# Performance work log

Hardware: AMD Instinct MI355X
Metric: run time of the kernel (lower is better)

## Reference

```python
import jax, jax.numpy as jnp
import numpy as np

SIZE = 64
B, NMAX = 8, 24


def setup_inputs() -> dict:
    key = jax.random.key(0)
    ks = jax.random.split(key, 8)
    # valid boxes: top-left in [0,400), width/height in [10,210)
    xy = jax.random.uniform(ks[0], (B, NMAX, 2)) * 400.0
    wh = jax.random.uniform(ks[1], (B, NMAX, 2)) * 200.0 + 10.0
    bboxes = jnp.concatenate([xy, xy + wh], axis=-1)  # [B,N,4] (x1,y1,x2,y2)
    num_obj = jax.random.randint(ks[2], (B,), 2, NMAX + 1)
    conv1_w = jax.random.normal(ks[3], (64, 2, 5, 5)) * 0.1
    conv1_b = jnp.zeros((64,), jnp.float32)
    conv2_w = jax.random.normal(ks[4], (32, 64, 5, 5)) * 0.05
    conv2_b = jnp.zeros((32,), jnp.float32)
    lin_w = jax.random.normal(ks[5], (5408, 4800)) * 0.01
    lin_b = jnp.zeros((4800,), jnp.float32)
    return dict(bboxes=bboxes, num_obj=num_obj, conv1_w=conv1_w, conv1_b=conv1_b,
                conv2_w=conv2_w, conv2_b=conv2_b, lin_w=lin_w, lin_b=lin_b)


def _pair_indices(num_obj):
    # ragged pair construction on host; num_obj is an integer constant input
    n = np.asarray(num_obj)
    bs, is_, js = [], [], []
    for b in range(n.shape[0]):
        ii, jj = np.triu_indices(int(n[b]), k=1)
        bs.append(np.full(ii.shape, b, dtype=np.int32))
        is_.append(ii.astype(np.int32))
        js.append(jj.astype(np.int32))
    return np.concatenate(bs), np.concatenate(is_), np.concatenate(js)


def _get_sp(boxA, boxB):
    # DRG-style spatial map: rescale both boxes into the union-box frame
    # (aspect preserving, shorter axis centered), rasterize as binary masks.
    # boxA, boxB: [M,4] -> [M,2,64,64]
    u1 = jnp.minimum(boxA[:, 0], boxB[:, 0])
    v1 = jnp.minimum(boxA[:, 1], boxB[:, 1])
    u2 = jnp.maximum(boxA[:, 2], boxB[:, 2])
    v2 = jnp.maximum(boxA[:, 3], boxB[:, 3])
    w = u2 - u1
    h = v2 - v1
    scale = (SIZE - 1.0) / jnp.maximum(jnp.maximum(w, h), 1e-6)
    offx = jnp.where(h >= w, (SIZE - 1.0 - w * scale) * 0.5, 0.0)
    offy = jnp.where(w > h, (SIZE - 1.0 - h * scale) * 0.5, 0.0)

    xs = jnp.arange(SIZE, dtype=jnp.float32)[None, None, :]
    ys = jnp.arange(SIZE, dtype=jnp.float32)[None, :, None]

    def rast(box):
        x1 = jnp.round((box[:, 0] - u1) * scale + offx)[:, None, None]
        y1 = jnp.round((box[:, 1] - v1) * scale + offy)[:, None, None]
        x2 = jnp.round((box[:, 2] - u1) * scale + offx)[:, None, None]
        y2 = jnp.round((box[:, 3] - v1) * scale + offy)[:, None, None]
        m = (xs >= x1) & (xs <= x2) & (ys >= y1) & (ys <= y2)
        return m.astype(jnp.float32)

    return jnp.stack([rast(boxA), rast(boxB)], axis=1)


def _conv(x, w, b):
    y = jax.lax.conv_general_dilated(x, w, (1, 1), 'VALID',
                                     dimension_numbers=('NCHW', 'OIHW', 'NCHW'))
    return y + b[None, :, None, None]


def _pool(x):
    return jax.lax.reduce_window(x, -jnp.inf, jax.lax.max,
                                 (1, 1, 2, 2), (1, 1, 2, 2), 'VALID')


def reference(bboxes, num_obj, conv1_w, conv1_b, conv2_w, conv2_b, lin_w, lin_b):
    bi, ii, ji = _pair_indices(num_obj)
    boxA = bboxes[bi, ii]                       # [M,4]
    boxB = bboxes[bi, ji]                       # [M,4]
    sp = _get_sp(boxA, boxB)                    # [M,2,64,64]
    x = jax.nn.relu(_conv(sp, conv1_w, conv1_b))   # [M,64,60,60]
    x = _pool(x)                                   # [M,64,30,30]
    x = jax.nn.relu(_conv(x, conv2_w, conv2_b))    # [M,32,26,26]
    x = _pool(x)                                   # [M,32,13,13]
    x = x.reshape(x.shape[0], -1)                  # [M,5408]
    feat = jax.nn.relu(x @ lin_w + lin_b)          # [M,4800]
    slicing = jnp.stack([jnp.asarray(bi), jnp.asarray(ii), jnp.asarray(ji)],
                        axis=1).astype(jnp.float32)  # [M,3]
    return feat, slicing
```

## Files before the change

### kernel.cpp

```cpp
#include <hip/hip_runtime.h>
#include <hip/hip_bf16.h>

typedef __attribute__((ext_vector_type(8))) short short8;
typedef __attribute__((ext_vector_type(4))) float f32x4;

__device__ inline unsigned short f2bf(float x) {
  unsigned u = __float_as_uint(x);
  unsigned rounding = 0x7FFFu + ((u >> 16) & 1u);
  return (unsigned short)((u + rounding) >> 16);
}
__device__ inline float bf2f(unsigned short u) {
  return __uint_as_float(((unsigned)u) << 16);
}
__device__ inline void gload_lds16(const void* g, void* l) {
  __builtin_amdgcn_global_load_lds(
      (const __attribute__((address_space(1))) unsigned int*)g,
      (__attribute__((address_space(3))) unsigned int*)l, 16, 0, 0);
}

#define KPAD 5440
#define NPAD 4864

__global__ void prep_pairs(const float* __restrict__ bboxes,
                           const int* __restrict__ num_obj, int M,
                           int* __restrict__ pairTab,
                           float* __restrict__ slicing) {
  __shared__ int cum[9];
  if (threadIdx.x == 0) {
    int c = 0; cum[0] = 0;
    for (int b = 0; b < 8; b++) { int n = num_obj[b]; c += n*(n-1)/2; cum[b+1] = c; }
  }
  __syncthreads();
  for (int m = threadIdx.x; m < M; m += blockDim.x) {
    int b = 0;
    while (b < 7 && m >= cum[b+1]) b++;
    int p = m - cum[b];
    int n = num_obj[b];
    int i = 0, rem = p;
    while (rem >= (n - 1 - i)) { rem -= (n - 1 - i); i++; }
    int j = i + 1 + rem;
    const float* A = bboxes + (b*24 + i)*4;
    const float* Bb = bboxes + (b*24 + j)*4;
    float ax1=A[0], ay1=A[1], ax2=A[2], ay2=A[3];
    float bx1=Bb[0], by1=Bb[1], bx2=Bb[2], by2=Bb[3];
    float u1 = fminf(ax1,bx1), v1 = fminf(ay1,by1);
    float u2 = fmaxf(ax2,bx2), v2 = fmaxf(ay2,by2);
    float w = u2-u1, h = v2-v1;
    float scale = 63.0f / fmaxf(fmaxf(w,h), 1e-6f);
    float offx = (h >= w) ? __fmul_rn(63.0f - __fmul_rn(w,scale), 0.5f) : 0.0f;
    float offy = (w > h)  ? __fmul_rn(63.0f - __fmul_rn(h,scale), 0.5f) : 0.0f;
    int* t = pairTab + m*8;
    t[0] = (int)rintf(__fadd_rn(__fmul_rn(ax1-u1, scale), offx));
    t[1] = (int)rintf(__fadd_rn(__fmul_rn(ay1-v1, scale), offy));
    t[2] = (int)rintf(__fadd_rn(__fmul_rn(ax2-u1, scale), offx));
    t[3] = (int)rintf(__fadd_rn(__fmul_rn(ay2-v1, scale), offy));
    t[4] = (int)rintf(__fadd_rn(__fmul_rn(bx1-u1, scale), offx));
    t[5] = (int)rintf(__fadd_rn(__fmul_rn(by1-v1, scale), offy));
    t[6] = (int)rintf(__fadd_rn(__fmul_rn(bx2-u1, scale), offx));
    t[7] = (int)rintf(__fadd_rn(__fmul_rn(by2-v1, scale), offy));
    slicing[m*3+0] = (float)b;
    slicing[m*3+1] = (float)i;
    slicing[m*3+2] = (float)j;
  }
}

__global__ void prep_tables(const float* __restrict__ w1, const float* __restrict__ w2,
                            float* __restrict__ T, unsigned short* __restrict__ W2A) {
  int idx = blockIdx.x*256 + threadIdx.x;
  if (idx < 86528) {
    int o = idx & 63;
    int t = idx >> 6;
    int rxi = t % 26; t /= 26;
    int ryi = t % 26;
    int c = t / 26;
    int ky0 = ryi/5, ky1 = ryi%5, kx0 = rxi/5, kx1 = rxi%5;
    float s = 0.f;
    for (int ky = ky0; ky <= ky1; ky++)
      for (int kx = kx0; kx <= kx1; kx++)
        s += w1[((o*2 + c)*5 + ky)*5 + kx];
    T[idx] = s;
  } else if (idx < 86528 + 51200) {
    int i = idx - 86528;
    int j = i & 7, ln = (i>>3) & 63;
    int mtk = i >> 9;
    int mt = mtk & 1, kk = mtk >> 1;
    int oc = mt*16 + (ln & 15);
    int k = kk*32 + ((ln>>4)<<3) + j;
    int halfk = k/800, r = k%800;
    int kyx = r >> 5, icl = r & 31;
    int ic = halfk*32 + icl, ky = kyx/5, kx = kyx%5;
    W2A[i] = f2bf(w2[((oc*64 + ic)*5 + ky)*5 + kx]);
  }
}

__global__ __launch_bounds__(256) void prep_wt(const float* __restrict__ lw,
                                               unsigned short* __restrict__ Wt) {
  __shared__ unsigned short tile[64][65];
  int k0 = blockIdx.x*64, n0 = blockIdx.y*64;
  for (int i = threadIdx.x; i < 64*64; i += 256) {
    int r = i >> 6, cdx = i & 63;
    int k = k0 + r, n = n0 + cdx;
    float v = (k < 5408) ? lw[(size_t)k*4800 + n] : 0.f;
    tile[r][cdx] = f2bf(v);
  }
  __syncthreads();
  for (int i = threadIdx.x; i < 64*64; i += 256) {
    int r = i >> 6, cdx = i & 63;
    int n = n0 + r, k = k0 + cdx;
    Wt[(size_t)n*KPAD + k] = tile[cdx][r];
  }
}

__global__ __launch_bounds__(256) void pair_conv(
    const int* __restrict__ pairTab, const float* __restrict__ T,
    const unsigned short* __restrict__ W2A, const float* __restrict__ b1,
    const float* __restrict__ b2, unsigned short* __restrict__ X) {
  __shared__ unsigned short p1[28800];
  __shared__ unsigned char rIdx[4][64];
  int m = blockIdx.x;
  int tid = threadIdx.x, lane = tid & 63, wid = tid >> 6;
  const int* pt = pairTab + m*8;

  if (tid < 240) {
    int q = tid % 60, which = tid / 60;
    int lo, hi;
    if (which == 0)      { lo = pt[1]; hi = pt[3]; }
    else if (which == 1) { lo = pt[5]; hi = pt[7]; }
    else if (which == 2) { lo = pt[0]; hi = pt[2]; }
    else                 { lo = pt[4]; hi = pt[6]; }
    int k0 = lo - q; if (k0 < 0) k0 = 0;
    int k1 = hi - q; if (k1 > 4) k1 = 4;
    rIdx[which][q] = (k0 > k1) ? (unsigned char)25 : (unsigned char)(k0*5 + k1);
  }

  int rowbase[11];
#pragma unroll
  for (int tt = 0; tt < 11; tt++) {
    int pos = (wid*11 + tt)*16 + (lane & 15);
    if (pos > 675) pos = 675;
    rowbase[tt] = (pos/26)*30 + (pos % 26);
  }
  f32x4 acc[11][2];
#pragma unroll
  for (int tt = 0; tt < 11; tt++) {
    acc[tt][0] = (f32x4){0.f,0.f,0.f,0.f};
    acc[tt][1] = (f32x4){0.f,0.f,0.f,0.f};
  }

  int icgl = lane >> 4;
  for (int half = 0; half < 2; half++) {
    __syncthreads();
    for (int item = tid; item < 3600; item += 256) {
      int pos = item >> 2;
      int icg = item & 3;
      int ic0 = half*32 + icg*8;
      int py = pos / 30, px = pos % 30;
      float best[8];
#pragma unroll
      for (int j = 0; j < 8; j++) best[j] = -1e30f;
#pragma unroll
      for (int d = 0; d < 4; d++) {
        int y = py*2 + (d>>1), x = px*2 + (d&1);
        int rya = rIdx[0][y], ryb = rIdx[1][y];
        int rxa = rIdx[2][x], rxb = rIdx[3][x];
        const float* Ta = T + (((rya)*26 + rxa)<<6) + ic0;
        const float* Tb = T + (((26 + ryb)*26 + rxb)<<6) + ic0;
        f32x4 a0 = *(const f32x4*)Ta, a1 = *(const f32x4*)(Ta+4);
        f32x4 c0 = *(const f32x4*)Tb, c1 = *(const f32x4*)(Tb+4);
#pragma unroll
        for (int j = 0; j < 4; j++) {
          best[j]   = fmaxf(best[j],   a0[j]+c0[j]);
          best[4+j] = fmaxf(best[4+j], a1[j]+c1[j]);
        }
      }
      short8 v;
#pragma unroll
      for (int j = 0; j < 8; j++)
        v[j] = (short)f2bf(fmaxf(best[j] + b1[ic0+j], 0.f));
      int byte = pos*64 + ((icg ^ ((pos>>1)&3))<<4);
      *(short8*)((char*)p1 + byte) = v;
    }
    __syncthreads();
    for (int kl = 0; kl < 25; kl++) {
      int kk = half*25 + kl;
      const unsigned short* wptr = W2A + ((size_t)(kk*2)*64 + lane)*8;
      short8 a0 = *(const short8*)wptr;
      short8 a1 = *(const short8*)(wptr + 512);
      int radd = (kl/5)*30 + (kl%5);
#pragma unroll
      for (int tt = 0; tt < 11; tt++) {
        int row = rowbase[tt] + radd;
        int byte = row*64 + ((icgl ^ ((row>>1)&3))<<4);
        short8 bv = *(const short8*)((const char*)p1 + byte);
        acc[tt][0] = __builtin_amdgcn_mfma_f32_16x16x32_bf16(a0, bv, acc[tt][0], 0, 0, 0);
        acc[tt][1] = __builtin_amdgcn_mfma_f32_16x16x32_bf16(a1, bv, acc[tt][1], 0, 0, 0);
      }
    }
  }
  __syncthreads();
#pragma unroll
  for (int tt = 0; tt < 11; tt++) {
    int pos = (wid*11 + tt)*16 + (lane & 15);
    if (pos <= 675) {
#pragma unroll
      for (int mt = 0; mt < 2; mt++)
#pragma unroll
        for (int r = 0; r < 4; r++) {
          int oc = mt*16 + ((lane>>4)<<2) + r;
          p1[oc*676 + pos] = f2bf(acc[tt][mt][r]);
        }
    }
  }
  __syncthreads();
  for (int f = tid; f < KPAD; f += 256) {
    unsigned short outv = 0;
    if (f < 5408) {
      int oc = f / 169, rem = f % 169;
      int py = rem / 13, px = rem % 13;
      const unsigned short* c2 = p1 + oc*676 + py*52 + px*2;
      float v = fmaxf(fmaxf(bf2f(c2[0]), bf2f(c2[1])), fmaxf(bf2f(c2[26]), bf2f(c2[27])));
      outv = f2bf(fmaxf(v + b2[oc], 0.f));
    }
    X[(size_t)m*KPAD + f] = outv;
  }
}

__global__ __launch_bounds__(256) void gemm_lin(
    const unsigned short* __restrict__ X, const unsigned short* __restrict__ Wt,
    const float* __restrict__ lin_b, float* __restrict__ P, float* __restrict__ out,
    int M, int Mpad, int splits) {
  __shared__ unsigned short As[2][4096];
  __shared__ unsigned short Bs[2][8192];
  int tid = threadIdx.x, lane = tid & 63, wid = tid >> 6;
  int m0 = blockIdx.x * 64, n0 = blockIdx.y * 128;
  int ks = blockIdx.z;
  int itBeg = (ks * 85) / splits, itEnd = ((ks + 1) * 85) / splits;
  int wm = wid >> 1, wn = wid & 1;

  f32x4 acc[2][4];
#pragma unroll
  for (int i = 0; i < 2; i++)
#pragma unroll
    for (int j = 0; j < 4; j++) acc[i][j] = (f32x4){0.f,0.f,0.f,0.f};

  int rsub = lane >> 3;
  int kslot = (lane & 7) ^ rsub;
  int kg = lane >> 4;

  auto stage = [&](int buf, int it) {
    size_t kof = (size_t)it * 64 + kslot * 8;
#pragma unroll
    for (int cc = 0; cc < 2; cc++) {
      int chunk = wid + cc*4;
      int gm = m0 + chunk*8 + rsub;
      gload_lds16(X + (size_t)gm*KPAD + kof, (char*)As[buf] + chunk*1024);
    }
#pragma unroll
    for (int cc = 0; cc < 4; cc++) {
      int chunk = wid + cc*4;
      int gn = n0 + chunk*8 + rsub;
      gload_lds16(Wt + (size_t)gn*KPAD + kof, (char*)Bs[buf] + chunk*1024);
    }
  };

  stage(0, itBeg);
  __syncthreads();
  int cur = 0;
  for (int it = itBeg; it < itEnd; ++it) {
    if (it + 1 < itEnd) stage(cur ^ 1, it + 1);
#pragma unroll
    for (int ksub = 0; ksub < 2; ++ksub) {
      int slot = ksub*4 + kg;
      short8 af[2], bfr[4];
#pragma unroll
      for (int mf = 0; mf < 2; mf++) {
        int r = wm*32 + mf*16 + (lane & 15);
        af[mf] = *(const short8*)((const char*)As[cur] + r*128 + ((slot ^ (lane&7))<<4));
      }
#pragma unroll
      for (int nf = 0; nf < 4; nf++) {
        int r = wn*64 + nf*16 + (lane & 15);
        bfr[nf] = *(const short8*)((const char*)Bs[cur] + r*128 + ((slot ^ (lane&7))<<4));
      }
#pragma unroll
      for (int mf = 0; mf < 2; mf++)
#pragma unroll
        for (int nf = 0; nf < 4; nf++)
          acc[mf][nf] = __builtin_amdgcn_mfma_f32_16x16x32_bf16(af[mf], bfr[nf], acc[mf][nf], 0, 0, 0);
    }
    __syncthreads();
    cur ^= 1;
  }

  if (splits == 1) {
#pragma unroll
    for (int mf = 0; mf < 2; mf++)
#pragma unroll
      for (int nf = 0; nf < 4; nf++) {
        int n = n0 + wn*64 + nf*16 + (lane & 15);
#pragma unroll
        for (int r = 0; r < 4; r++) {
          int mm = m0 + wm*32 + mf*16 + ((lane>>4)<<2) + r;
          if (mm < M && n < 4800)
            out[(size_t)mm*4800 + n] = fmaxf(acc[mf][nf][r] + lin_b[n], 0.f);
        }
      }
  } else {
    float* Pp = P + (size_t)ks * Mpad * NPAD;
#pragma unroll
    for (int mf = 0; mf < 2; mf++)
#pragma unroll
      for (int nf = 0; nf < 4; nf++) {
        int n = n0 + wn*64 + nf*16 + (lane & 15);
#pragma unroll
        for (int r = 0; r < 4; r++) {
          int mm = m0 + wm*32 + mf*16 + ((lane>>4)<<2) + r;
          Pp[(size_t)mm*NPAD + n] = acc[mf][nf][r];
        }
      }
  }
}

__global__ void reduce_out(const float* __restrict__ P, const float* __restrict__ lb,
                           float* __restrict__ out, int M, int Mpad, int splits) {
  int total = M * 1200;
  for (int idx = blockIdx.x*256 + threadIdx.x; idx < total; idx += gridDim.x*256) {
    int m = idx / 1200, q = idx - m*1200;
    int n = q * 4;
    f32x4 s = *(const f32x4*)(P + (size_t)m*NPAD + n);
    for (int sidx = 1; sidx < splits; sidx++)
      s += *(const f32x4*)(P + (size_t)sidx*Mpad*NPAD + (size_t)m*NPAD + n);
    f32x4 b = *(const f32x4*)(lb + n);
    f32x4 r;
#pragma unroll
    for (int j = 0; j < 4; j++) r[j] = fmaxf(s[j] + b[j], 0.f);
    *(f32x4*)(out + (size_t)m*4800 + n) = r;
  }
}

extern "C" void kernel_launch(void* const* d_in, const int* in_sizes, int n_in,
                              void* d_out, int out_size, void* d_ws, size_t ws_size,
                              hipStream_t stream) {
  const float* bboxes = (const float*)d_in[0];
  const int*   num_obj = (const int*)d_in[1];
  const float* w1 = (const float*)d_in[2];
  const float* b1 = (const float*)d_in[3];
  const float* w2 = (const float*)d_in[4];
  const float* b2 = (const float*)d_in[5];
  const float* lw = (const float*)d_in[6];
  const float* lb = (const float*)d_in[7];
  float* out = (float*)d_out;
  int M = out_size / 4803;
  int Mpad = (M + 63) & ~63;

  size_t fixed = 0;
  auto align512 = [](size_t x) { return (x + 511) & ~(size_t)511; };
  fixed += align512((size_t)M*8*4);
  fixed += align512((size_t)86528*4);
  fixed += align512((size_t)51200*2);
  fixed += align512((size_t)4800*KPAD*2);
  fixed += align512((size_t)Mpad*KPAD*2);
  int splits = 4;
  while (splits > 1 && fixed + align512((size_t)splits*Mpad*NPAD*4) > ws_size) splits >>= 1;

  char* ws = (char*)d_ws;
  size_t off = 0;
  auto alloc = [&](size_t bytes) {
    off = align512(off);
    char* p = ws + off;
    off += bytes;
    return p;
  };
  int* pairTab = (int*)alloc((size_t)M*8*4);
  float* T = (float*)alloc((size_t)86528*4);
  unsigned short* W2A = (unsigned short*)alloc((size_t)51200*2);
  unsigned short* Wt = (unsigned short*)alloc((size_t)4800*KPAD*2);
  unsigned short* X = (unsigned short*)alloc((size_t)Mpad*KPAD*2);
  float* P = (splits > 1) ? (float*)alloc((size_t)splits*Mpad*NPAD*4) : nullptr;

  prep_pairs<<<1, 256, 0, stream>>>(bboxes, num_obj, M, pairTab, out + (size_t)M*4800);
  prep_tables<<<(137728+255)/256, 256, 0, stream>>>(w1, w2, T, W2A);
  prep_wt<<<dim3(85, 75), 256, 0, stream>>>(lw, Wt);
  pair_conv<<<M, 256, 0, stream>>>(pairTab, T, W2A, b1, b2, X);
  gemm_lin<<<dim3(Mpad/64, 38, splits), 256, 0, stream>>>(X, Wt, lb, P, out, M, Mpad, splits);
  if (splits > 1)
    reduce_out<<<1024, 256, 0, stream>>>(P, lb, out, M, Mpad, splits);
}
```

Baseline: 278.7 us.

## Halve pair_conv LDS by processing conv2 input channels in four 16-channel passes

Result: slower. 472.8 us (+69.7%).

```diff
diff --git a/kernel.cpp b/kernel.cpp
--- a/kernel.cpp
+++ b/kernel.cpp
@@ -65,7 +65,7 @@
 }
 
 __global__ void prep_tables(const float* __restrict__ w1, const float* __restrict__ w2,
-                            float* __restrict__ T, unsigned short* __restrict__ W2A) {
+                            float* __restrict__ T, unsigned short* __restrict__ W2B) {
   int idx = blockIdx.x*256 + threadIdx.x;
   if (idx < 86528) {
     int o = idx & 63;
@@ -79,17 +79,22 @@
       for (int kx = kx0; kx <= kx1; kx++)
         s += w1[((o*2 + c)*5 + ky)*5 + kx];
     T[idx] = s;
-  } else if (idx < 86528 + 51200) {
+  } else if (idx < 86528 + 53248) {
     int i = idx - 86528;
-    int j = i & 7, ln = (i>>3) & 63;
-    int mtk = i >> 9;
-    int mt = mtk & 1, kk = mtk >> 1;
+    int j = i & 7;
+    int ln = (i >> 3) & 63;
+    int r1 = i >> 9;
+    int mt = r1 & 1;
+    int r2 = r1 >> 1;
+    int s = r2 % 13;
+    int pp = r2 / 13;
     int oc = mt*16 + (ln & 15);
-    int k = kk*32 + ((ln>>4)<<3) + j;
-    int halfk = k/800, r = k%800;
-    int kyx = r >> 5, icl = r & 31;
-    int ic = halfk*32 + icl, ky = kyx/5, kx = kyx%5;
-    W2A[i] = f2bf(w2[((oc*64 + ic)*5 + ky)*5 + kx]);
+    int q = ln >> 4;
+    int kyx = 2*s + (q >> 1);
+    int ic = pp*16 + ((q & 1) << 3) + j;
+    float val = 0.f;
+    if (kyx < 25) val = w2[((oc*64 + ic)*5 + kyx/5)*5 + (kyx%5)];
+    W2B[i] = f2bf(val);
   }
 }
 
@@ -111,11 +116,11 @@
   }
 }
 
-__global__ __launch_bounds__(256) void pair_conv(
+__global__ __launch_bounds__(256, 4) void pair_conv(
     const int* __restrict__ pairTab, const float* __restrict__ T,
-    const unsigned short* __restrict__ W2A, const float* __restrict__ b1,
+    const unsigned short* __restrict__ W2B, const float* __restrict__ b1,
     const float* __restrict__ b2, unsigned short* __restrict__ X) {
-  __shared__ unsigned short p1[28800];
+  __shared__ unsigned short p1[14400];
   __shared__ unsigned char rIdx[4][64];
   int m = blockIdx.x;
   int tid = threadIdx.x, lane = tid & 63, wid = tid >> 6;
@@ -147,13 +152,16 @@
     acc[tt][1] = (f32x4){0.f,0.f,0.f,0.f};
   }
 
-  int icgl = lane >> 4;
-  for (int half = 0; half < 2; half++) {
-    __syncthreads();
-    for (int item = tid; item < 3600; item += 256) {
-      int pos = item >> 2;
-      int icg = item & 3;
-      int ic0 = half*32 + icg*8;
+  int q = lane >> 4;
+  int qh = q >> 1;
+  int qs = q & 1;
+
+  for (int pp = 0; pp < 4; pp++) {
+    __syncthreads();
+    for (int item = tid; item < 1800; item += 256) {
+      int pos = item >> 1;
+      int icg = item & 1;
+      int ch0 = pp*16 + icg*8;
       int py = pos / 30, px = pos % 30;
       float best[8];
 #pragma unroll
@@ -163,8 +171,8 @@
         int y = py*2 + (d>>1), x = px*2 + (d&1);
         int rya = rIdx[0][y], ryb = rIdx[1][y];
         int rxa = rIdx[2][x], rxb = rIdx[3][x];
-        const float* Ta = T + (((rya)*26 + rxa)<<6) + ic0;
-        const float* Tb = T + (((26 + ryb)*26 + rxb)<<6) + ic0;
+        const float* Ta = T + (((rya)*26 + rxa)<<6) + ch0;
+        const float* Tb = T + (((26 + ryb)*26 + rxb)<<6) + ch0;
         f32x4 a0 = *(const f32x4*)Ta, a1 = *(const f32x4*)(Ta+4);
         f32x4 c0 = *(const f32x4*)Tb, c1 = *(const f32x4*)(Tb+4);
 #pragma unroll
@@ -176,53 +184,53 @@
       short8 v;
 #pragma unroll
       for (int j = 0; j < 8; j++)
-        v[j] = (short)f2bf(fmaxf(best[j] + b1[ic0+j], 0.f));
-      int byte = pos*64 + ((icg ^ ((pos>>1)&3))<<4);
+        v[j] = (short)f2bf(fmaxf(best[j] + b1[ch0+j], 0.f));
+      int byte = pos*32 + ((icg ^ ((pos>>2)&1))<<4);
       *(short8*)((char*)p1 + byte) = v;
     }
     __syncthreads();
-    for (int kl = 0; kl < 25; kl++) {
-      int kk = half*25 + kl;
-      const unsigned short* wptr = W2A + ((size_t)(kk*2)*64 + lane)*8;
+    const unsigned short* wbase = W2B + (size_t)(pp*13)*1024;
+    for (int s = 0; s < 13; s++) {
+      const unsigned short* wptr = wbase + (size_t)s*1024 + lane*8;
       short8 a0 = *(const short8*)wptr;
       short8 a1 = *(const short8*)(wptr + 512);
-      int radd = (kl/5)*30 + (kl%5);
+      int kyx = 2*s + qh; if (kyx > 24) kyx = 24;
+      int radd = (kyx/5)*30 + (kyx%5);
 #pragma unroll
       for (int tt = 0; tt < 11; tt++) {
         int row = rowbase[tt] + radd;
-        int byte = row*64 + ((icgl ^ ((row>>1)&3))<<4);
+        int byte = row*32 + ((qs ^ ((row>>2)&1))<<4);
         short8 bv = *(const short8*)((const char*)p1 + byte);
         acc[tt][0] = __builtin_amdgcn_mfma_f32_16x16x32_bf16(a0, bv, acc[tt][0], 0, 0, 0);
         acc[tt][1] = __builtin_amdgcn_mfma_f32_16x16x32_bf16(a1, bv, acc[tt][1], 0, 0, 0);
       }
     }
   }
-  __syncthreads();
-#pragma unroll
-  for (int tt = 0; tt < 11; tt++) {
-    int pos = (wid*11 + tt)*16 + (lane & 15);
-    if (pos <= 675) {
-#pragma unroll
-      for (int mt = 0; mt < 2; mt++)
+  for (int mt = 0; mt < 2; mt++) {
+    __syncthreads();
+#pragma unroll
+    for (int tt = 0; tt < 11; tt++) {
+      int pos = (wid*11 + tt)*16 + (lane & 15);
+      if (pos <= 675) {
 #pragma unroll
         for (int r = 0; r < 4; r++) {
-          int oc = mt*16 + ((lane>>4)<<2) + r;
-          p1[oc*676 + pos] = f2bf(acc[tt][mt][r]);
+          int ocl = (q<<2) + r;
+          p1[ocl*676 + pos] = f2bf(acc[tt][mt][r]);
         }
-    }
-  }
-  __syncthreads();
-  for (int f = tid; f < KPAD; f += 256) {
-    unsigned short outv = 0;
-    if (f < 5408) {
-      int oc = f / 169, rem = f % 169;
+      }
+    }
+    __syncthreads();
+    for (int f = tid; f < 2704; f += 256) {
+      int ocl = f / 169, rem = f % 169;
+      int oc = mt*16 + ocl;
       int py = rem / 13, px = rem % 13;
-      const unsigned short* c2 = p1 + oc*676 + py*52 + px*2;
+      const unsigned short* c2 = p1 + ocl*676 + py*52 + px*2;
       float v = fmaxf(fmaxf(bf2f(c2[0]), bf2f(c2[1])), fmaxf(bf2f(c2[26]), bf2f(c2[27])));
-      outv = f2bf(fmaxf(v + b2[oc], 0.f));
-    }
-    X[(size_t)m*KPAD + f] = outv;
-  }
+      X[(size_t)m*KPAD + oc*169 + rem] = f2bf(fmaxf(v + b2[oc], 0.f));
+    }
+  }
+  for (int f = 5408 + tid; f < KPAD; f += 256)
+    X[(size_t)m*KPAD + f] = 0;
 }
 
 __global__ __launch_bounds__(256) void gemm_lin(
@@ -325,8 +333,8 @@
                            float* __restrict__ out, int M, int Mpad, int splits) {
   int total = M * 1200;
   for (int idx = blockIdx.x*256 + threadIdx.x; idx < total; idx += gridDim.x*256) {
-    int m = idx / 1200, q = idx - m*1200;
-    int n = q * 4;
+    int m = idx / 1200, qq = idx - m*1200;
+    int n = qq * 4;
     f32x4 s = *(const f32x4*)(P + (size_t)m*NPAD + n);
     for (int sidx = 1; sidx < splits; sidx++)
       s += *(const f32x4*)(P + (size_t)sidx*Mpad*NPAD + (size_t)m*NPAD + n);
@@ -357,7 +365,7 @@
   auto align512 = [](size_t x) { return (x + 511) & ~(size_t)511; };
   fixed += align512((size_t)M*8*4);
   fixed += align512((size_t)86528*4);
-  fixed += align512((size_t)51200*2);
+  fixed += align512((size_t)53248*2);
   fixed += align512((size_t)4800*KPAD*2);
   fixed += align512((size_t)Mpad*KPAD*2);
   int splits = 4;
@@ -373,15 +381,15 @@
   };
   int* pairTab = (int*)alloc((size_t)M*8*4);
   float* T = (float*)alloc((size_t)86528*4);
-  unsigned short* W2A = (unsigned short*)alloc((size_t)51200*2);
+  unsigned short* W2B = (unsigned short*)alloc((size_t)53248*2);
   unsigned short* Wt = (unsigned short*)alloc((size_t)4800*KPAD*2);
   unsigned short* X = (unsigned short*)alloc((size_t)Mpad*KPAD*2);
   float* P = (splits > 1) ? (float*)alloc((size_t)splits*Mpad*NPAD*4) : nullptr;
 
   prep_pairs<<<1, 256, 0, stream>>>(bboxes, num_obj, M, pairTab, out + (size_t)M*4800);
-  prep_tables<<<(137728+255)/256, 256, 0, stream>>>(w1, w2, T, W2A);
+  prep_tables<<<(86528+53248+255)/256, 256, 0, stream>>>(w1, w2, T, W2B);
   prep_wt<<<dim3(85, 75), 256, 0, stream>>>(lw, Wt);
-  pair_conv<<<M, 256, 0, stream>>>(pairTab, T, W2A, b1, b2, X);
+  pair_conv<<<M, 256, 0, stream>>>(pairTab, T, W2B, b1, b2, X);
   gemm_lin<<<dim3(Mpad/64, 38, splits), 256, 0, stream>>>(X, Wt, lb, P, out, M, Mpad, splits);
   if (splits > 1)
     reduce_out<<<1024, 256, 0, stream>>>(P, lb, out, M, Mpad, splits);
```
